# Kernel tuning notes

Hardware: AMD Instinct MI355X
Metric: run time of the kernel (lower is better)

## Reference

```python
import jax, jax.numpy as jnp
import numpy as np

N_NODES = 20000
N_EDGES = 320000
N_GRAPHS = 64
SEQ = 20
SCALAR = 16
EMB = 32
HID = 128
HEADS = 4
IN_DIM = SCALAR + 5 * EMB  # 176
NEG_SLOPE = 0.2


def masked_mean_embed(table, idx):
    # table: [V, EMB], idx: [N, L] with 0 = padding
    emb = table[idx]                                  # [N, L, EMB]
    mask = (idx != 0).astype(emb.dtype)[..., None]    # [N, L, 1]
    return (emb * mask).sum(axis=1) / (mask.sum(axis=1) + 1e-9)


def gat_conv(x, src, dst, W, att_src, att_dst, bias, heads, out_ch):
    # PyG GATConv (add_self_loops already applied to src/dst), concat heads.
    N = x.shape[0]
    xw = (x @ W).reshape(N, heads, out_ch)            # [N, H, C]
    a_src = (xw * att_src).sum(-1)                    # [N, H]
    a_dst = (xw * att_dst).sum(-1)                    # [N, H]
    e = jax.nn.leaky_relu(a_src[src] + a_dst[dst], NEG_SLOPE)  # [E, H]
    e_max = jax.ops.segment_max(e, dst, num_segments=N)
    e_max = jnp.where(jnp.isfinite(e_max), e_max, 0.0)
    ex = jnp.exp(e - e_max[dst])                      # [E, H]
    denom = jax.ops.segment_sum(ex, dst, num_segments=N)
    alpha = ex / (denom[dst] + 1e-16)                 # [E, H]
    msg = xw[src] * alpha[:, :, None]                 # [E, H, C]
    out = jax.ops.segment_sum(msg, dst, num_segments=N)
    return out.reshape(N, heads * out_ch) + bias


def setup_inputs() -> dict:
    key = jax.random.key(0)
    ks = jax.random.split(key, 24)
    s = 0.05
    inp = {
        "x_scalar": jax.random.normal(ks[0], (N_NODES, SCALAR), jnp.float32),
        "x_opcode": jax.random.randint(ks[1], (N_NODES, SEQ), 0, 256),
        "x_source": jax.random.randint(ks[2], (N_NODES, SEQ), 0, 512),
        "x_sink": jax.random.randint(ks[3], (N_NODES, SEQ), 0, 512),
        "x_string_manip": jax.random.randint(ks[4], (N_NODES, SEQ), 0, 128),
        "x_payload": jax.random.randint(ks[5], (N_NODES, SEQ), 0, 1024),
        "edge_index": jax.random.randint(ks[6], (2, N_EDGES), 0, N_NODES),
        "batch": jnp.sort(jax.random.randint(ks[7], (N_NODES,), 0, N_GRAPHS)),
        # embedding tables (row 0 = padding; masked out anyway)
        "emb_opcode": jax.random.normal(ks[8], (256, EMB)) * s,
        "emb_source": jax.random.normal(ks[9], (512, EMB)) * s,
        "emb_sink": jax.random.normal(ks[10], (512, EMB)) * s,
        "emb_string": jax.random.normal(ks[11], (128, EMB)) * s,
        "emb_payload": jax.random.normal(ks[12], (1024, EMB)) * s,
        "ln_gamma": jnp.ones((IN_DIM,), jnp.float32),
        "ln_beta": jnp.zeros((IN_DIM,), jnp.float32),
        "W1": jax.random.normal(ks[13], (IN_DIM, HEADS * HID)) * s,
        "att_src1": jax.random.normal(ks[14], (HEADS, HID)) * s,
        "att_dst1": jax.random.normal(ks[15], (HEADS, HID)) * s,
        "b1": jnp.zeros((HEADS * HID,), jnp.float32),
        "W2": jax.random.normal(ks[16], (HEADS * HID, HID)) * s,
        "att_src2": jax.random.normal(ks[17], (1, HID)) * s,
        "att_dst2": jax.random.normal(ks[18], (1, HID)) * s,
        "b2": jnp.zeros((HID,), jnp.float32),
        "cls_w1": jax.random.normal(ks[19], (HID, HID // 2)) * s,
        "cls_b1": jnp.zeros((HID // 2,), jnp.float32),
        "cls_w2": jax.random.normal(ks[20], (HID // 2, 2)) * s,
        "cls_b2": jnp.zeros((2,), jnp.float32),
    }
    return inp


def reference(x_scalar, x_opcode, x_source, x_sink, x_string_manip, x_payload,
              edge_index, batch,
              emb_opcode, emb_source, emb_sink, emb_string, emb_payload,
              ln_gamma, ln_beta,
              W1, att_src1, att_dst1, b1,
              W2, att_src2, att_dst2, b2,
              cls_w1, cls_b1, cls_w2, cls_b2):
    feats = jnp.concatenate([
        x_scalar,
        masked_mean_embed(emb_opcode, x_opcode),
        masked_mean_embed(emb_source, x_source),
        masked_mean_embed(emb_sink, x_sink),
        masked_mean_embed(emb_string, x_string_manip),
        masked_mean_embed(emb_payload, x_payload),
    ], axis=1)  # [N, 176]
    mu = feats.mean(-1, keepdims=True)
    var = ((feats - mu) ** 2).mean(-1, keepdims=True)
    h = (feats - mu) / jnp.sqrt(var + 1e-5) * ln_gamma + ln_beta

    # add self loops (PyG GATConv default)
    loops = jnp.arange(N_NODES, dtype=edge_index.dtype)
    src = jnp.concatenate([edge_index[0], loops])
    dst = jnp.concatenate([edge_index[1], loops])

    x = jax.nn.elu(gat_conv(h, src, dst, W1, att_src1, att_dst1, b1, HEADS, HID))
    x = jax.nn.elu(gat_conv(x, src, dst, W2, att_src2, att_dst2, b2, 1, HID))

    pooled = jax.ops.segment_max(x, batch, num_segments=N_GRAPHS)  # [G, HID]
    hcls = jax.nn.relu(pooled @ cls_w1 + cls_b1)
    return hcls @ cls_w2 + cls_b2  # [G, 2]
```

## Files before the change

### kernel.cpp

```cpp
#include <hip/hip_runtime.h>
#include <hip/hip_bf16.h>
#include <math.h>

#define N_NODES 20000
#define N_EDGES 320000
#define N_GRAPHS 64
#define SEQ 20
#define SCALAR 16
#define EMB 32
#define HID 128
#define IN_DIM 176
#define TOT_EDGES (N_EDGES + N_NODES)
#define CHUNK_SMALL 10000
#define POOL_SLICES 32

typedef _Float16 half8v __attribute__((ext_vector_type(8)));
typedef float f32x4 __attribute__((ext_vector_type(4)));
#define LO_SCALE 2048.0f
#define LO_INV (1.0f / 2048.0f)

#define PB2_ELEMS (16 * 8 * 64 * 8)
#define PB1_ELEMS (4 * 6 * 8 * 64 * 8)

__device__ inline float readlane_f(float v, int l) {
  return __uint_as_float(__builtin_amdgcn_readlane(__float_as_uint(v), l));
}
__device__ inline int readlane_i(int v, int l) {
  return __builtin_amdgcn_readlane(v, l);
}
__device__ inline float leaky(float e) { return e >= 0.f ? e : 0.2f * e; }
__device__ inline float elu(float v) { return v > 0.f ? v : expf(v) - 1.f; }

__global__ __launch_bounds__(256) void wasd_kernel(
    const float* __restrict__ W1, const float* __restrict__ att_s,
    const float* __restrict__ att_d, float* __restrict__ was4,
    float* __restrict__ wad4) {
  int lane = threadIdx.x & 63;
  int k = blockIdx.x * 4 + (threadIdx.x >> 6);
  if (k >= IN_DIM) return;
  const float* wrow = W1 + (size_t)k * 512;
  float s[4], d[4];
#pragma unroll
  for (int hh = 0; hh < 4; ++hh) {
    float w0 = wrow[hh * 128 + lane], w1 = wrow[hh * 128 + 64 + lane];
    float a0 = att_s[hh * 128 + lane], a1 = att_s[hh * 128 + 64 + lane];
    float c0 = att_d[hh * 128 + lane], c1 = att_d[hh * 128 + 64 + lane];
    s[hh] = w0 * a0 + w1 * a1;
    d[hh] = w0 * c0 + w1 * c1;
  }
  for (int off = 1; off < 64; off <<= 1) {
#pragma unroll
    for (int hh = 0; hh < 4; ++hh) {
      s[hh] += __shfl_xor(s[hh], off);
      d[hh] += __shfl_xor(d[hh], off);
    }
  }
  if (lane == 0) {
    *(float4*)&was4[k * 4] = make_float4(s[0], s[1], s[2], s[3]);
    *(float4*)&wad4[k * 4] = make_float4(d[0], d[1], d[2], d[3]);
  }
}

__global__ __launch_bounds__(256) void feats_ln_kernel(
    const float* __restrict__ xs,
    const int* __restrict__ i0, const int* __restrict__ i1,
    const int* __restrict__ i2, const int* __restrict__ i3,
    const int* __restrict__ i4,
    const float* __restrict__ t0, const float* __restrict__ t1,
    const float* __restrict__ t2, const float* __restrict__ t3,
    const float* __restrict__ t4,
    const float* __restrict__ gamma, const float* __restrict__ beta,
    const float* __restrict__ was4, const float* __restrict__ wad4,
    float* __restrict__ hout, float* __restrict__ a_s,
    float* __restrict__ a_d) {
  int lane = threadIdx.x & 63;
  int w = threadIdx.x >> 6;
  int n = blockIdx.x * 4 + w;
  if (n >= N_NODES) return;
  __shared__ int sidx[4][100];
  {
    int j = lane;
    int tab = j / 20, l = j - tab * 20;
    const int* ip = tab == 0 ? i0 : tab == 1 ? i1 : tab == 2 ? i2 : i3;
    sidx[w][j] = ip[n * SEQ + l];
    if (lane < 36) {
      int j2 = 64 + lane;
      int tab2 = j2 / 20, l2 = j2 - tab2 * 20;
      const int* ip2 = tab2 == 3 ? i3 : i4;
      sidx[w][j2] = ip2[n * SEQ + l2];
    }
  }
  bool l48 = lane < 48;
  float f0, f1, f2 = 0.f;
  if (lane < SCALAR) {
    f0 = xs[n * SCALAR + lane];
  } else {
    int tt = lane - SCALAR, tab = tt >> 5, d = tt & 31;
    const float* tp = tab == 0 ? t0 : t1;
    float sum = 0.f, cnt = 0.f;
#pragma unroll
    for (int l = 0; l < SEQ; ++l) {
      int id = sidx[w][tab * 20 + l];
      if (id != 0) { sum += tp[id * EMB + d]; cnt += 1.f; }
    }
    f0 = sum / (cnt + 1e-9f);
  }
  {
    int tt = 48 + lane, tab = tt >> 5, d = tt & 31;
    const float* tp = tab == 1 ? t1 : tab == 2 ? t2 : t3;
    float sum = 0.f, cnt = 0.f;
#pragma unroll
    for (int l = 0; l < SEQ; ++l) {
      int id = sidx[w][tab * 20 + l];
      if (id != 0) { sum += tp[id * EMB + d]; cnt += 1.f; }
    }
    f1 = sum / (cnt + 1e-9f);
  }
  if (l48) {
    int tt = 112 + lane, tab = tt >> 5, d = tt & 31;
    const float* tp = tab == 3 ? t3 : t4;
    float sum = 0.f, cnt = 0.f;
#pragma unroll
    for (int l = 0; l < SEQ; ++l) {
      int id = sidx[w][tab * 20 + l];
      if (id != 0) { sum += tp[id * EMB + d]; cnt += 1.f; }
    }
    f2 = sum / (cnt + 1e-9f);
  }
  float s = f0 + f1 + f2;
  for (int off = 1; off < 64; off <<= 1) s += __shfl_xor(s, off);
  float mu = s / (float)IN_DIM;
  float v = (f0 - mu) * (f0 - mu) + (f1 - mu) * (f1 - mu) +
            (l48 ? (f2 - mu) * (f2 - mu) : 0.f);
  for (int off = 1; off < 64; off <<= 1) v += __shfl_xor(v, off);
  float rstd = 1.0f / sqrtf(v / (float)IN_DIM + 1e-5f);
  float hv0 = (f0 - mu) * rstd * gamma[lane] + beta[lane];
  float hv1 = (f1 - mu) * rstd * gamma[64 + lane] + beta[64 + lane];
  float hv2 = l48 ? (f2 - mu) * rstd * gamma[128 + lane] + beta[128 + lane] : 0.f;
  float* hr = hout + (size_t)n * IN_DIM;
  hr[lane] = hv0;
  hr[64 + lane] = hv1;
  if (l48) hr[128 + lane] = hv2;

  const float4* wsv = (const float4*)was4;
  const float4* wdv = (const float4*)wad4;
  float4 wsa = wsv[lane], wsb = wsv[64 + lane];
  float4 wsc = l48 ? wsv[128 + lane] : make_float4(0.f, 0.f, 0.f, 0.f);
  float4 wda = wdv[lane], wdb = wdv[64 + lane];
  float4 wdc = l48 ? wdv[128 + lane] : make_float4(0.f, 0.f, 0.f, 0.f);
  float ps0 = hv0 * wsa.x + hv1 * wsb.x + hv2 * wsc.x;
  float ps1 = hv0 * wsa.y + hv1 * wsb.y + hv2 * wsc.y;
  float ps2 = hv0 * wsa.z + hv1 * wsb.z + hv2 * wsc.z;
  float ps3 = hv0 * wsa.w + hv1 * wsb.w + hv2 * wsc.w;
  float pd0 = hv0 * wda.x + hv1 * wdb.x + hv2 * wdc.x;
  float pd1 = hv0 * wda.y + hv1 * wdb.y + hv2 * wdc.y;
  float pd2 = hv0 * wda.z + hv1 * wdb.z + hv2 * wdc.z;
  float pd3 = hv0 * wda.w + hv1 * wdb.w + hv2 * wdc.w;
  for (int off = 1; off < 64; off <<= 1) {
    ps0 += __shfl_xor(ps0, off); ps1 += __shfl_xor(ps1, off);
    ps2 += __shfl_xor(ps2, off); ps3 += __shfl_xor(ps3, off);
    pd0 += __shfl_xor(pd0, off); pd1 += __shfl_xor(pd1, off);
    pd2 += __shfl_xor(pd2, off); pd3 += __shfl_xor(pd3, off);
  }
  if (lane == 0) {
    *(float4*)&a_s[n * 4] = make_float4(ps0, ps1, ps2, ps3);
    *(float4*)&a_d[n * 4] = make_float4(pd0, pd1, pd2, pd3);
  }
}

__global__ void count_kernel(const int* __restrict__ edge_index,
                             int* __restrict__ cnt, int E, int N) {
  int i = blockIdx.x * blockDim.x + threadIdx.x;
  if (i < E) {
    atomicAdd(&cnt[edge_index[E + i]], 1);
  } else if (i < E + N) {
    atomicAdd(&cnt[i - E], 1);
  }
}

__global__ __launch_bounds__(256) void prefix_kernel(const int* __restrict__ cnt,
                                                     int* __restrict__ indptr,
                                                     int n, int total) {
  __shared__ int ssum[256];
  int t = threadIdx.x;
  int per = (n + 255) / 256;
  int beg = t * per, end = min(beg + per, n);
  int s = 0;
  for (int i = beg; i < end; ++i) s += cnt[i];
  ssum[t] = s;
  __syncthreads();
  if (t == 0) {
    int run = 0;
    for (int i = 0; i < 256; ++i) { int v = ssum[i]; ssum[i] = run; run += v; }
  }
  __syncthreads();
  int run = ssum[t];
  for (int i = beg; i < end; ++i) { indptr[i] = run; run += cnt[i]; }
  if (t == 0) indptr[n] = total;
}

__global__ void scatter_kernel(const int* __restrict__ edge_index,
                               const int* __restrict__ indptr,
                               int* __restrict__ cursor,
                               int* __restrict__ srcs, int E, int N) {
  int i = blockIdx.x * blockDim.x + threadIdx.x;
  int s, d;
  if (i < E) { s = edge_index[i]; d = edge_index[E + i]; }
  else if (i < E + N) { s = i - E; d = s; }
  else return;
  int pos = indptr[d] + atomicAdd(&cursor[d], 1);
  srcs[pos] = s;
}

__global__ __launch_bounds__(256) void agg1h_kernel(
    const float* __restrict__ h, const float* __restrict__ a_src,
    const float* __restrict__ a_dst, const int* __restrict__ indptr,
    const int* __restrict__ srcs, float* __restrict__ aggh,
    int n0, int nM) {
  int lane = threadIdx.x & 63;
  int ln = blockIdx.x * 4 + (threadIdx.x >> 6);
  if (ln >= nM) return;
  int n = n0 + ln;
  int beg = indptr[n], end = indptr[n + 1];
  int deg = end - beg;
  float4 ad = *(const float4*)&a_dst[n * 4];
  bool l48 = lane < 48;
  float acc[4][3] = {};

  auto body = [&](int s, float al0, float al1, float al2, float al3) {
    const float* r = h + (size_t)s * IN_DIM;
    float v0 = r[lane];
    float v1 = r[64 + lane];
    float v2 = l48 ? r[128 + lane] : 0.f;
    acc[0][0] += al0 * v0; acc[0][1] += al0 * v1; acc[0][2] += al0 * v2;
    acc[1][0] += al1 * v0; acc[1][1] += al1 * v1; acc[1][2] += al1 * v2;
    acc[2][0] += al2 * v0; acc[2][1] += al2 * v1; acc[2][2] += al2 * v2;
    acc[3][0] += al3 * v0; acc[3][1] += al3 * v1; acc[3][2] += al3 * v2;
  };

  if (deg <= 64) {
    int j = beg + lane;
    int s = 0;
    float e0 = -INFINITY, e1 = -INFINITY, e2 = -INFINITY, e3 = -INFINITY;
    if (j < end) {
      s = srcs[j];
      float4 as = *(const float4*)&a_src[s * 4];
      e0 = leaky(as.x + ad.x); e1 = leaky(as.y + ad.y);
      e2 = leaky(as.z + ad.z); e3 = leaky(as.w + ad.w);
    }
    float m0 = e0, m1 = e1, m2 = e2, m3 = e3;
    for (int off = 1; off < 64; off <<= 1) {
      m0 = fmaxf(m0, __shfl_xor(m0, off)); m1 = fmaxf(m1, __shfl_xor(m1, off));
      m2 = fmaxf(m2, __shfl_xor(m2, off)); m3 = fmaxf(m3, __shfl_xor(m3, off));
    }
    float x0 = (j < end) ? expf(e0 - m0) : 0.f;
    float x1 = (j < end) ? expf(e1 - m1) : 0.f;
    float x2 = (j < end) ? expf(e2 - m2) : 0.f;
    float x3 = (j < end) ? expf(e3 - m3) : 0.f;
    float d0 = x0, d1 = x1, d2 = x2, d3 = x3;
    for (int off = 1; off < 64; off <<= 1) {
      d0 += __shfl_xor(d0, off); d1 += __shfl_xor(d1, off);
      d2 += __shfl_xor(d2, off); d3 += __shfl_xor(d3, off);
    }
    float al0 = x0 / (d0 + 1e-16f), al1 = x1 / (d1 + 1e-16f);
    float al2 = x2 / (d2 + 1e-16f), al3 = x3 / (d3 + 1e-16f);
    int jj = 0;
    for (; jj + 2 <= deg; jj += 2) {
      int sa = readlane_i(s, jj), sb = readlane_i(s, jj + 1);
      float a0 = readlane_f(al0, jj), a1 = readlane_f(al1, jj);
      float a2 = readlane_f(al2, jj), a3 = readlane_f(al3, jj);
      float b0 = readlane_f(al0, jj + 1), b1 = readlane_f(al1, jj + 1);
      float b2 = readlane_f(al2, jj + 1), b3 = readlane_f(al3, jj + 1);
      body(sa, a0, a1, a2, a3);
      body(sb, b0, b1, b2, b3);
    }
    if (jj < deg) {
      int sa = readlane_i(s, jj);
      body(sa, readlane_f(al0, jj), readlane_f(al1, jj),
           readlane_f(al2, jj), readlane_f(al3, jj));
    }
  } else {
    float m0 = -INFINITY, m1 = -INFINITY, m2 = -INFINITY, m3 = -INFINITY;
    for (int j0 = beg; j0 < end; j0 += 64) {
      int j = j0 + lane;
      if (j < end) {
        int s = srcs[j];
        float4 as = *(const float4*)&a_src[s * 4];
        m0 = fmaxf(m0, leaky(as.x + ad.x)); m1 = fmaxf(m1, leaky(as.y + ad.y));
        m2 = fmaxf(m2, leaky(as.z + ad.z)); m3 = fmaxf(m3, leaky(as.w + ad.w));
      }
    }
    for (int off = 1; off < 64; off <<= 1) {
      m0 = fmaxf(m0, __shfl_xor(m0, off)); m1 = fmaxf(m1, __shfl_xor(m1, off));
      m2 = fmaxf(m2, __shfl_xor(m2, off)); m3 = fmaxf(m3, __shfl_xor(m3, off));
    }
    float d0 = 0.f, d1 = 0.f, d2 = 0.f, d3 = 0.f;
    for (int j0 = beg; j0 < end; j0 += 64) {
      int j = j0 + lane;
      if (j < end) {
        int s = srcs[j];
        float4 as = *(const float4*)&a_src[s * 4];
        d0 += expf(leaky(as.x + ad.x) - m0); d1 += expf(leaky(as.y + ad.y) - m1);
        d2 += expf(leaky(as.z + ad.z) - m2); d3 += expf(leaky(as.w + ad.w) - m3);
      }
    }
    for (int off = 1; off < 64; off <<= 1) {
      d0 += __shfl_xor(d0, off); d1 += __shfl_xor(d1, off);
      d2 += __shfl_xor(d2, off); d3 += __shfl_xor(d3, off);
    }
    float r0 = 1.f / (d0 + 1e-16f), r1 = 1.f / (d1 + 1e-16f);
    float r2 = 1.f / (d2 + 1e-16f), r3 = 1.f / (d3 + 1e-16f);
    for (int j0 = beg; j0 < end; j0 += 64) {
      int jn = min(64, end - j0);
      int j = j0 + lane;
      int s = 0;
      float al0 = 0.f, al1 = 0.f, al2 = 0.f, al3 = 0.f;
      if (j < end) {
        s = srcs[j];
        float4 as = *(const float4*)&a_src[s * 4];
        al0 = expf(leaky(as.x + ad.x) - m0) * r0;
        al1 = expf(leaky(as.y + ad.y) - m1) * r1;
        al2 = expf(leaky(as.z + ad.z) - m2) * r2;
        al3 = expf(leaky(as.w + ad.w) - m3) * r3;
      }
      for (int jj = 0; jj < jn; ++jj) {
        body(readlane_i(s, jj), readlane_f(al0, jj), readlane_f(al1, jj),
             readlane_f(al2, jj), readlane_f(al3, jj));
      }
    }
  }

  size_t base = (size_t)ln * (4 * IN_DIM);
#pragma unroll
  for (int hh = 0; hh < 4; ++hh) {
    aggh[base + hh * IN_DIM + lane] = acc[hh][0];
    aggh[base + hh * IN_DIM + 64 + lane] = acc[hh][1];
    if (l48) aggh[base + hh * IN_DIM + 128 + lane] = acc[hh][2];
  }
}

__global__ __launch_bounds__(256) void pack_w2_kernel(
    const float* __restrict__ W2, _Float16* __restrict__ PBh,
    _Float16* __restrict__ PBl) {
  int t = blockIdx.x * 256 + threadIdx.x;
  int lane = t & 63, wi = t >> 6;
  int r = lane & 15, g = lane >> 4;
  int ks = wi >> 3, ntile = wi & 7;
  int col = ntile * 16 + r;
  size_t o = ((size_t)wi * 64 + lane) * 8;
#pragma unroll
  for (int j = 0; j < 8; ++j) {
    int k = ks * 32 + g * 8 + j;
    float v = W2[(size_t)k * 128 + col];
    _Float16 h = (_Float16)v;
    PBh[o + j] = h;
    PBl[o + j] = (_Float16)((v - (float)h) * LO_SCALE);
  }
}

__global__ __launch_bounds__(256) void pack_w1_kernel(
    const float* __restrict__ W1, _Float16* __restrict__ PBh,
    _Float16* __restrict__ PBl) {
  int t = blockIdx.x * 256 + threadIdx.x;
  int lane = t & 63, wi = t >> 6;
  int r = lane & 15, g = lane >> 4;
  int ntile = wi & 7, rem = wi >> 3;
  int ks = rem % 6, hh = rem / 6;
  int col = hh * 128 + ntile * 16 + r;
  size_t o = ((size_t)wi * 64 + lane) * 8;
#pragma unroll
  for (int j = 0; j < 8; ++j) {
    int k = ks * 32 + g * 8 + j;
    float v = (k < IN_DIM) ? W1[(size_t)k * 512 + col] : 0.f;
    _Float16 h = (_Float16)v;
    PBh[o + j] = h;
    PBl[o + j] = (_Float16)((v - (float)h) * LO_SCALE);
  }
}

__global__ __launch_bounds__(256) void gemm_head_mfma_kernel(
    const float* __restrict__ aggh, const half8v* __restrict__ PBh,
    const half8v* __restrict__ PBl, const float* __restrict__ b1,
    float* __restrict__ out1, int M, int n0) {
  int lane = threadIdx.x & 63;
  int wid = (blockIdx.x * 256 + threadIdx.x) >> 6;
  int colhalf = wid & 1;
  int hh = (wid >> 1) & 3;
  int rg = wid >> 3;
  int rows0 = rg * 32;
  if (rows0 >= M) return;
  int r = lane & 15, g = lane >> 4;
  f32x4 acc[2][4] = {};
  f32x4 accm[2][4] = {};
  const float* a0 = aggh + ((size_t)(rows0 + r) * 4 + hh) * IN_DIM;
  const float* a1 = aggh + ((size_t)(rows0 + 16 + r) * 4 + hh) * IN_DIM;
#pragma unroll 2
  for (int ks = 0; ks < 6; ++ks) {
    int kg = ks * 32 + g * 8;
    int koff = (kg + 8 <= IN_DIM) ? kg : 0;
    half8v ah[2], al[2];
#pragma unroll
    for (int mt = 0; mt < 2; ++mt) {
      const float* ap = (mt ? a1 : a0) + koff;
      float av[8];
      *(float4*)&av[0] = *(const float4*)(ap);
      *(float4*)&av[4] = *(const float4*)(ap + 4);
#pragma unroll
      for (int j = 0; j < 8; ++j) {
        _Float16 hv = (_Float16)av[j];
        ah[mt][j] = hv;
        al[mt][j] = (_Float16)((av[j] - (float)hv) * LO_SCALE);
      }
    }
    const half8v* bh = PBh + (size_t)(((hh * 6 + ks) * 8 + colhalf * 4) * 64) + lane;
    const half8v* bl = PBl + (size_t)(((hh * 6 + ks) * 8 + colhalf * 4) * 64) + lane;
#pragma unroll
    for (int nt = 0; nt < 4; ++nt) {
      half8v bhv = bh[nt * 64], blv = bl[nt * 64];
#pragma unroll
      for (int mt = 0; mt < 2; ++mt) {
        accm[mt][nt] = __builtin_amdgcn_mfma_f32_16x16x32_f16(al[mt], bhv, accm[mt][nt], 0, 0, 0);
        accm[mt][nt] = __builtin_amdgcn_mfma_f32_16x16x32_f16(ah[mt], blv, accm[mt][nt], 0, 0, 0);
        acc[mt][nt]  = __builtin_amdgcn_mfma_f32_16x16x32_f16(ah[mt], bhv, acc[mt][nt], 0, 0, 0);
      }
    }
  }
#pragma unroll
  for (int nt = 0; nt < 4; ++nt) {
    int col = hh * 128 + colhalf * 64 + nt * 16 + r;
    float bb = b1[col];
#pragma unroll
    for (int mt = 0; mt < 2; ++mt) {
#pragma unroll
      for (int i = 0; i < 4; ++i) {
        int row = rows0 + mt * 16 + g * 4 + i;
        if (row < M)
          out1[(size_t)(n0 + row) * 512 + col] =
              elu(acc[mt][nt][i] + accm[mt][nt][i] * LO_INV + bb);
      }
    }
  }
}

__global__ __launch_bounds__(256) void gemm2att_mfma_kernel(
    const float* __restrict__ A, const half8v* __restrict__ PBh,
    const half8v* __restrict__ PBl, const float* __restrict__ att_s,
    const float* __restrict__ att_d, float* __restrict__ C,
    float* __restrict__ a_s, float* __restrict__ a_d, int M) {
  int lane = threadIdx.x & 63;
  int wid = (blockIdx.x * 256 + threadIdx.x) >> 6;
  int colhalf = wid & 1;
  int rg = wid >> 1;
  int row0 = rg * 16;
  if (row0 >= M) return;
  int r = lane & 15, g = lane >> 4;
  const float* arow = A + (size_t)(row0 + r) * 512 + g * 8;
  f32x4 acc[4] = {};
  f32x4 accm[4] = {};
#pragma unroll 2
  for (int ks = 0; ks < 16; ++ks) {
    float av[8];
    *(float4*)&av[0] = *(const float4*)(arow + ks * 32);
    *(float4*)&av[4] = *(const float4*)(arow + ks * 32 + 4);
    half8v ah, al;
#pragma unroll
    for (int j = 0; j < 8; ++j) {
      _Float16 hv = (_Float16)av[j];
      ah[j] = hv;
      al[j] = (_Float16)((av[j] - (float)hv) * LO_SCALE);
    }
    const half8v* bh = PBh + (size_t)((ks * 8 + colhalf * 4) * 64) + lane;
    const half8v* bl = PBl + (size_t)((ks * 8 + colhalf * 4) * 64) + lane;
#pragma unroll
    for (int nt = 0; nt < 4; ++nt) {
      half8v bhv = bh[nt * 64], blv = bl[nt * 64];
      accm[nt] = __builtin_amdgcn_mfma_f32_16x16x32_f16(al, bhv, accm[nt], 0, 0, 0);
      accm[nt] = __builtin_amdgcn_mfma_f32_16x16x32_f16(ah, blv, accm[nt], 0, 0, 0);
      acc[nt]  = __builtin_amdgcn_mfma_f32_16x16x32_f16(ah, bhv, acc[nt], 0, 0, 0);
    }
  }
  float ps[4] = {0.f, 0.f, 0.f, 0.f}, pd[4] = {0.f, 0.f, 0.f, 0.f};
#pragma unroll
  for (int nt = 0; nt < 4; ++nt) {
    int col = colhalf * 64 + nt * 16 + r;
    float as_ = att_s[col], ad_ = att_d[col];
#pragma unroll
    for (int i = 0; i < 4; ++i) {
      float v = acc[nt][i] + accm[nt][i] * LO_INV;
      int row = row0 + g * 4 + i;
      C[(size_t)row * 128 + col] = v;
      ps[i] += v * as_;
      pd[i] += v * ad_;
    }
  }
#pragma unroll
  for (int i = 0; i < 4; ++i) {
    for (int off = 1; off < 16; off <<= 1) {
      ps[i] += __shfl_xor(ps[i], off);
      pd[i] += __shfl_xor(pd[i], off);
    }
  }
  if (r == 0) {
#pragma unroll
    for (int i = 0; i < 4; ++i) {
      atomicAdd(&a_s[row0 + g * 4 + i], ps[i]);
      atomicAdd(&a_d[row0 + g * 4 + i], pd[i]);
    }
  }
}

__global__ __launch_bounds__(256) void agg2_kernel(
    const float* __restrict__ xw, const float* __restrict__ a_src,
    const float* __restrict__ a_dst, const int* __restrict__ indptr,
    const int* __restrict__ srcs, const float* __restrict__ bias,
    float* __restrict__ out) {
  int lane = threadIdx.x & 63;
  int n = blockIdx.x * 4 + (threadIdx.x >> 6);
  if (n >= N_NODES) return;
  int beg = indptr[n], end = indptr[n + 1];
  int deg = end - beg;
  float adn = a_dst[n];
  int half = lane >> 5, l32 = lane & 31;
  float4 acc = make_float4(0.f, 0.f, 0.f, 0.f);

  auto pairs = [&](int s, float al, int jn) {
    int jj = 0;
    for (; jj + 2 <= jn; jj += 2) {
      int sa = readlane_i(s, jj), sb = readlane_i(s, jj + 1);
      float aa = readlane_f(al, jj), ab = readlane_f(al, jj + 1);
      int sh = half ? sb : sa;
      float ahx = half ? ab : aa;
      float4 v = *(const float4*)&xw[(size_t)sh * HID + l32 * 4];
      acc.x += ahx * v.x; acc.y += ahx * v.y; acc.z += ahx * v.z; acc.w += ahx * v.w;
    }
    if (jj < jn) {
      int sa = readlane_i(s, jj);
      float ahx = half ? 0.f : readlane_f(al, jj);
      float4 v = *(const float4*)&xw[(size_t)sa * HID + l32 * 4];
      acc.x += ahx * v.x; acc.y += ahx * v.y; acc.z += ahx * v.z; acc.w += ahx * v.w;
    }
  };

  if (deg <= 64) {
    int j = beg + lane;
    int s = 0;
    float e = -INFINITY;
    if (j < end) { s = srcs[j]; e = leaky(a_src[s] + adn); }
    float m = e;
    for (int off = 1; off < 64; off <<= 1) m = fmaxf(m, __shfl_xor(m, off));
    float x = (j < end) ? expf(e - m) : 0.f;
    float d = x;
    for (int off = 1; off < 64; off <<= 1) d += __shfl_xor(d, off);
    float al = x / (d + 1e-16f);
    pairs(s, al, deg);
  } else {
    float m = -INFINITY;
    for (int j0 = beg; j0 < end; j0 += 64) {
      int j = j0 + lane;
      if (j < end) m = fmaxf(m, leaky(a_src[srcs[j]] + adn));
    }
    for (int off = 1; off < 64; off <<= 1) m = fmaxf(m, __shfl_xor(m, off));
    float d = 0.f;
    for (int j0 = beg; j0 < end; j0 += 64) {
      int j = j0 + lane;
      if (j < end) d += expf(leaky(a_src[srcs[j]] + adn) - m);
    }
    for (int off = 1; off < 64; off <<= 1) d += __shfl_xor(d, off);
    float rd = 1.f / (d + 1e-16f);
    for (int j0 = beg; j0 < end; j0 += 64) {
      int jn = min(64, end - j0);
      int j = j0 + lane;
      int s = 0;
      float al = 0.f;
      if (j < end) {
        s = srcs[j];
        al = expf(leaky(a_src[s] + adn) - m) * rd;
      }
      pairs(s, al, jn);
    }
  }

  acc.x += __shfl_xor(acc.x, 32); acc.y += __shfl_xor(acc.y, 32);
  acc.z += __shfl_xor(acc.z, 32); acc.w += __shfl_xor(acc.w, 32);
  if (half == 0) {
    float4 b = *(const float4*)&bias[l32 * 4];
    float4 o;
    o.x = elu(acc.x + b.x); o.y = elu(acc.y + b.y);
    o.z = elu(acc.z + b.z); o.w = elu(acc.w + b.w);
    *(float4*)&out[(size_t)n * HID + l32 * 4] = o;
  }
}

__global__ void gstart_kernel(const int* __restrict__ batch,
                              int* __restrict__ gstarts, int N, int G) {
  int t = threadIdx.x;
  if (t > G) return;
  int lo = 0, hi = N;
  while (lo < hi) {
    int mid = (lo + hi) >> 1;
    if (batch[mid] < t) lo = mid + 1; else hi = mid;
  }
  gstarts[t] = lo;
}

__global__ __launch_bounds__(HID) void pool_part_kernel(
    const float* __restrict__ out2, const int* __restrict__ gstarts,
    float* __restrict__ part) {
  int g = blockIdx.x, s = blockIdx.y, t = threadIdx.x;
  int beg = gstarts[g], end = gstarts[g + 1];
  int len = end - beg;
  int b0 = beg + (int)(((long long)len * s) / POOL_SLICES);
  int b1 = beg + (int)(((long long)len * (s + 1)) / POOL_SLICES);
  float m = -INFINITY;
  for (int n = b0; n < b1; ++n) m = fmaxf(m, out2[(size_t)n * HID + t]);
  part[((size_t)g * POOL_SLICES + s) * HID + t] = m;
}

__global__ __launch_bounds__(HID) void pool_reduce_kernel(
    const float* __restrict__ part, float* __restrict__ pooled) {
  int g = blockIdx.x, t = threadIdx.x;
  float m = -INFINITY;
#pragma unroll
  for (int s = 0; s < POOL_SLICES; ++s)
    m = fmaxf(m, part[((size_t)g * POOL_SLICES + s) * HID + t]);
  pooled[g * HID + t] = m;
}

__global__ __launch_bounds__(HID) void cls_kernel(const float* __restrict__ pooled,
                                                  const float* __restrict__ w1,
                                                  const float* __restrict__ b1,
                                                  const float* __restrict__ w2,
                                                  const float* __restrict__ b2,
                                                  float* __restrict__ out) {
  int g = blockIdx.x, t = threadIdx.x;
  __shared__ float sp[HID], sh1[HID / 2];
  sp[t] = pooled[g * HID + t];
  __syncthreads();
  if (t < HID / 2) {
    float s = b1[t];
    for (int k = 0; k < HID; ++k) s += sp[k] * w1[k * (HID / 2) + t];
    sh1[t] = fmaxf(s, 0.f);
  }
  __syncthreads();
  if (t < 2) {
    float o = b2[t];
    for (int k = 0; k < HID / 2; ++k) o += sh1[k] * w2[k * 2 + t];
    out[g * 2 + t] = o;
  }
}

extern "C" void kernel_launch(void* const* d_in, const int* in_sizes, int n_in,
                              void* d_out, int out_size, void* d_ws, size_t ws_size,
                              hipStream_t stream) {
  const float* x_scalar = (const float*)d_in[0];
  const int* x_opcode   = (const int*)d_in[1];
  const int* x_source   = (const int*)d_in[2];
  const int* x_sink     = (const int*)d_in[3];
  const int* x_string   = (const int*)d_in[4];
  const int* x_payload  = (const int*)d_in[5];
  const int* edge_index = (const int*)d_in[6];
  const int* batch      = (const int*)d_in[7];
  const float* emb_opcode = (const float*)d_in[8];
  const float* emb_source = (const float*)d_in[9];
  const float* emb_sink   = (const float*)d_in[10];
  const float* emb_string = (const float*)d_in[11];
  const float* emb_payload= (const float*)d_in[12];
  const float* ln_gamma = (const float*)d_in[13];
  const float* ln_beta  = (const float*)d_in[14];
  const float* W1       = (const float*)d_in[15];
  const float* att_src1 = (const float*)d_in[16];
  const float* att_dst1 = (const float*)d_in[17];
  const float* b1       = (const float*)d_in[18];
  const float* W2       = (const float*)d_in[19];
  const float* att_src2 = (const float*)d_in[20];
  const float* att_dst2 = (const float*)d_in[21];
  const float* b2       = (const float*)d_in[22];
  const float* cls_w1   = (const float*)d_in[23];
  const float* cls_b1   = (const float*)d_in[24];
  const float* cls_w2   = (const float*)d_in[25];
  const float* cls_b2   = (const float*)d_in[26];

  auto total_bytes = [&](int chunk) -> size_t {
    size_t f = (size_t)N_NODES * IN_DIM + (size_t)chunk * 4 * IN_DIM +
               (size_t)N_NODES * 512 + (size_t)N_NODES * HID +
               N_NODES * 4 * 2 + N_NODES * 2 + IN_DIM * 4 * 2 + N_GRAPHS * HID;
    size_t ii = (N_NODES + 1) + N_NODES * 2 + TOT_EDGES + (N_GRAPHS + 1);
    size_t f16b = (size_t)2 * (PB2_ELEMS + PB1_ELEMS) * sizeof(_Float16) + 32;
    size_t poolb = (size_t)N_GRAPHS * POOL_SLICES * HID * 4 + 32;
    return f * 4 + ii * 4 + f16b + poolb + 256;
  };
  int chunk = (ws_size >= total_bytes(N_NODES)) ? N_NODES : CHUNK_SMALL;

  float* h      = (float*)d_ws;
  float* aggh   = h + (size_t)N_NODES * IN_DIM;
  float* out1   = aggh + (size_t)chunk * 4 * IN_DIM;
  float* out2   = out1 + (size_t)N_NODES * 512;
  float* a1s    = out2 + (size_t)N_NODES * HID;
  float* a1d    = a1s + N_NODES * 4;
  float* was4   = a1d + N_NODES * 4;
  float* wad4   = was4 + IN_DIM * 4;
  float* pooled = wad4 + IN_DIM * 4;
  int* indptr = (int*)(pooled + N_GRAPHS * HID);
  int* cnt    = indptr + (N_NODES + 1);
  int* cursor = cnt + N_NODES;
  float* a2s  = (float*)(cursor + N_NODES);
  float* a2d  = a2s + N_NODES;
  int* srcs   = (int*)(a2d + N_NODES);
  int* gstarts= srcs + TOT_EDGES;
  uintptr_t pal = ((uintptr_t)(gstarts + N_GRAPHS + 1) + 15) & ~(uintptr_t)15;
  _Float16* PB2h = (_Float16*)pal;
  _Float16* PB2l = PB2h + PB2_ELEMS;
  _Float16* PB1h = PB2l + PB2_ELEMS;
  _Float16* PB1l = PB1h + PB1_ELEMS;
  uintptr_t ppal = ((uintptr_t)(PB1l + PB1_ELEMS) + 15) & ~(uintptr_t)15;
  float* pool_part = (float*)ppal;
  float* xw2  = h;

  hipMemsetAsync(cnt, 0, 4 * N_NODES * sizeof(int), stream);

  const int NB4 = (N_NODES + 3) / 4;

  wasd_kernel<<<(IN_DIM + 3) / 4, 256, 0, stream>>>(W1, att_src1, att_dst1, was4, wad4);

  feats_ln_kernel<<<NB4, 256, 0, stream>>>(
      x_scalar, x_opcode, x_source, x_sink, x_string, x_payload,
      emb_opcode, emb_source, emb_sink, emb_string, emb_payload,
      ln_gamma, ln_beta, was4, wad4, h, a1s, a1d);

  int nthreads = TOT_EDGES;
  count_kernel<<<(nthreads + 255) / 256, 256, 0, stream>>>(edge_index, cnt, N_EDGES, N_NODES);
  prefix_kernel<<<1, 256, 0, stream>>>(cnt, indptr, N_NODES, TOT_EDGES);
  scatter_kernel<<<(nthreads + 255) / 256, 256, 0, stream>>>(edge_index, indptr, cursor, srcs, N_EDGES, N_NODES);

  pack_w1_kernel<<<48, 256, 0, stream>>>(W1, PB1h, PB1l);
  pack_w2_kernel<<<32, 256, 0, stream>>>(W2, PB2h, PB2l);

  for (int n0 = 0; n0 < N_NODES; n0 += chunk) {
    int nM = min(chunk, N_NODES - n0);
    agg1h_kernel<<<(nM + 3) / 4, 256, 0, stream>>>(h, a1s, a1d, indptr, srcs, aggh, n0, nM);
    int rgs = (nM + 31) / 32;
    gemm_head_mfma_kernel<<<rgs * 2, 256, 0, stream>>>(
        aggh, (const half8v*)PB1h, (const half8v*)PB1l, b1, out1, nM, n0);
  }

  gemm2att_mfma_kernel<<<((N_NODES + 15) / 16 * 2 + 3) / 4, 256, 0, stream>>>(
      out1, (const half8v*)PB2h, (const half8v*)PB2l, att_src2, att_dst2,
      xw2, a2s, a2d, N_NODES);

  agg2_kernel<<<NB4, 256, 0, stream>>>(xw2, a2s, a2d, indptr, srcs, b2, out2);

  gstart_kernel<<<1, 128, 0, stream>>>(batch, gstarts, N_NODES, N_GRAPHS);
  pool_part_kernel<<<dim3(N_GRAPHS, POOL_SLICES), HID, 0, stream>>>(out2, gstarts, pool_part);
  pool_reduce_kernel<<<N_GRAPHS, HID, 0, stream>>>(pool_part, pooled);
  cls_kernel<<<N_GRAPHS, HID, 0, stream>>>(pooled, cls_w1, cls_b1, cls_w2, cls_b2, (float*)d_out);
}
```

Baseline: 390.8 us.

## Merge setup kernels, parallelize prefix scan, and shrink GEMM wave tiles

```diff
diff --git a/kernel.cpp b/kernel.cpp
--- a/kernel.cpp
+++ b/kernel.cpp
@@ -31,33 +31,69 @@
 __device__ inline float leaky(float e) { return e >= 0.f ? e : 0.2f * e; }
 __device__ inline float elu(float v) { return v > 0.f ? v : expf(v) - 1.f; }
 
-__global__ __launch_bounds__(256) void wasd_kernel(
-    const float* __restrict__ W1, const float* __restrict__ att_s,
-    const float* __restrict__ att_d, float* __restrict__ was4,
-    float* __restrict__ wad4) {
-  int lane = threadIdx.x & 63;
-  int k = blockIdx.x * 4 + (threadIdx.x >> 6);
-  if (k >= IN_DIM) return;
-  const float* wrow = W1 + (size_t)k * 512;
-  float s[4], d[4];
-#pragma unroll
-  for (int hh = 0; hh < 4; ++hh) {
-    float w0 = wrow[hh * 128 + lane], w1 = wrow[hh * 128 + 64 + lane];
-    float a0 = att_s[hh * 128 + lane], a1 = att_s[hh * 128 + 64 + lane];
-    float c0 = att_d[hh * 128 + lane], c1 = att_d[hh * 128 + 64 + lane];
-    s[hh] = w0 * a0 + w1 * a1;
-    d[hh] = w0 * c0 + w1 * c1;
-  }
-  for (int off = 1; off < 64; off <<= 1) {
+__global__ __launch_bounds__(256) void setup_kernel(
+    const float* __restrict__ W1, const float* __restrict__ att_s1,
+    const float* __restrict__ att_d1, const float* __restrict__ W2,
+    float* __restrict__ was4, float* __restrict__ wad4,
+    _Float16* __restrict__ PB1h, _Float16* __restrict__ PB1l,
+    _Float16* __restrict__ PB2h, _Float16* __restrict__ PB2l) {
+  int b = blockIdx.x;
+  if (b < 44) {
+    int lane = threadIdx.x & 63;
+    int k = b * 4 + (threadIdx.x >> 6);
+    if (k >= IN_DIM) return;
+    const float* wrow = W1 + (size_t)k * 512;
+    float s[4], d[4];
 #pragma unroll
     for (int hh = 0; hh < 4; ++hh) {
-      s[hh] += __shfl_xor(s[hh], off);
-      d[hh] += __shfl_xor(d[hh], off);
-    }
-  }
-  if (lane == 0) {
-    *(float4*)&was4[k * 4] = make_float4(s[0], s[1], s[2], s[3]);
-    *(float4*)&wad4[k * 4] = make_float4(d[0], d[1], d[2], d[3]);
+      float w0 = wrow[hh * 128 + lane], w1 = wrow[hh * 128 + 64 + lane];
+      float a0 = att_s1[hh * 128 + lane], a1 = att_s1[hh * 128 + 64 + lane];
+      float c0 = att_d1[hh * 128 + lane], c1 = att_d1[hh * 128 + 64 + lane];
+      s[hh] = w0 * a0 + w1 * a1;
+      d[hh] = w0 * c0 + w1 * c1;
+    }
+    for (int off = 1; off < 64; off <<= 1) {
+#pragma unroll
+      for (int hh = 0; hh < 4; ++hh) {
+        s[hh] += __shfl_xor(s[hh], off);
+        d[hh] += __shfl_xor(d[hh], off);
+      }
+    }
+    if (lane == 0) {
+      *(float4*)&was4[k * 4] = make_float4(s[0], s[1], s[2], s[3]);
+      *(float4*)&wad4[k * 4] = make_float4(d[0], d[1], d[2], d[3]);
+    }
+  } else if (b < 92) {
+    int t = (b - 44) * 256 + threadIdx.x;
+    int lane = t & 63, wi = t >> 6;
+    int r = lane & 15, g = lane >> 4;
+    int ntile = wi & 7, rem = wi >> 3;
+    int ks = rem % 6, hh = rem / 6;
+    int col = hh * 128 + ntile * 16 + r;
+    size_t o = ((size_t)wi * 64 + lane) * 8;
+#pragma unroll
+    for (int j = 0; j < 8; ++j) {
+      int k = ks * 32 + g * 8 + j;
+      float v = (k < IN_DIM) ? W1[(size_t)k * 512 + col] : 0.f;
+      _Float16 h = (_Float16)v;
+      PB1h[o + j] = h;
+      PB1l[o + j] = (_Float16)((v - (float)h) * LO_SCALE);
+    }
+  } else {
+    int t = (b - 92) * 256 + threadIdx.x;
+    int lane = t & 63, wi = t >> 6;
+    int r = lane & 15, g = lane >> 4;
+    int ks = wi >> 3, ntile = wi & 7;
+    int col = ntile * 16 + r;
+    size_t o = ((size_t)wi * 64 + lane) * 8;
+#pragma unroll
+    for (int j = 0; j < 8; ++j) {
+      int k = ks * 32 + g * 8 + j;
+      float v = W2[(size_t)k * 128 + col];
+      _Float16 h = (_Float16)v;
+      PB2h[o + j] = h;
+      PB2l[o + j] = (_Float16)((v - (float)h) * LO_SCALE);
+    }
   }
 }
 
@@ -178,23 +214,24 @@
   }
 }
 
-__global__ __launch_bounds__(256) void prefix_kernel(const int* __restrict__ cnt,
-                                                     int* __restrict__ indptr,
-                                                     int n, int total) {
-  __shared__ int ssum[256];
+__global__ __launch_bounds__(1024) void prefix_kernel(const int* __restrict__ cnt,
+                                                      int* __restrict__ indptr,
+                                                      int n, int total) {
+  __shared__ int ss[1024];
   int t = threadIdx.x;
-  int per = (n + 255) / 256;
+  int per = (n + 1023) / 1024;
   int beg = t * per, end = min(beg + per, n);
   int s = 0;
   for (int i = beg; i < end; ++i) s += cnt[i];
-  ssum[t] = s;
+  ss[t] = s;
   __syncthreads();
-  if (t == 0) {
-    int run = 0;
-    for (int i = 0; i < 256; ++i) { int v = ssum[i]; ssum[i] = run; run += v; }
-  }
-  __syncthreads();
-  int run = ssum[t];
+  for (int off = 1; off < 1024; off <<= 1) {
+    int v = (t >= off) ? ss[t - off] : 0;
+    __syncthreads();
+    ss[t] += v;
+    __syncthreads();
+  }
+  int run = ss[t] - s;
   for (int i = beg; i < end; ++i) { indptr[i] = run; run += cnt[i]; }
   if (t == 0) indptr[n] = total;
 }
@@ -339,45 +376,6 @@
   }
 }
 
-__global__ __launch_bounds__(256) void pack_w2_kernel(
-    const float* __restrict__ W2, _Float16* __restrict__ PBh,
-    _Float16* __restrict__ PBl) {
-  int t = blockIdx.x * 256 + threadIdx.x;
-  int lane = t & 63, wi = t >> 6;
-  int r = lane & 15, g = lane >> 4;
-  int ks = wi >> 3, ntile = wi & 7;
-  int col = ntile * 16 + r;
-  size_t o = ((size_t)wi * 64 + lane) * 8;
-#pragma unroll
-  for (int j = 0; j < 8; ++j) {
-    int k = ks * 32 + g * 8 + j;
-    float v = W2[(size_t)k * 128 + col];
-    _Float16 h = (_Float16)v;
-    PBh[o + j] = h;
-    PBl[o + j] = (_Float16)((v - (float)h) * LO_SCALE);
-  }
-}
-
-__global__ __launch_bounds__(256) void pack_w1_kernel(
-    const float* __restrict__ W1, _Float16* __restrict__ PBh,
-    _Float16* __restrict__ PBl) {
-  int t = blockIdx.x * 256 + threadIdx.x;
-  int lane = t & 63, wi = t >> 6;
-  int r = lane & 15, g = lane >> 4;
-  int ntile = wi & 7, rem = wi >> 3;
-  int ks = rem % 6, hh = rem / 6;
-  int col = hh * 128 + ntile * 16 + r;
-  size_t o = ((size_t)wi * 64 + lane) * 8;
-#pragma unroll
-  for (int j = 0; j < 8; ++j) {
-    int k = ks * 32 + g * 8 + j;
-    float v = (k < IN_DIM) ? W1[(size_t)k * 512 + col] : 0.f;
-    _Float16 h = (_Float16)v;
-    PBh[o + j] = h;
-    PBl[o + j] = (_Float16)((v - (float)h) * LO_SCALE);
-  }
-}
-
 __global__ __launch_bounds__(256) void gemm_head_mfma_kernel(
     const float* __restrict__ aggh, const half8v* __restrict__ PBh,
     const half8v* __restrict__ PBl, const float* __restrict__ b1,
@@ -387,42 +385,35 @@
   int colhalf = wid & 1;
   int hh = (wid >> 1) & 3;
   int rg = wid >> 3;
-  int rows0 = rg * 32;
+  int rows0 = rg * 16;
   if (rows0 >= M) return;
   int r = lane & 15, g = lane >> 4;
-  f32x4 acc[2][4] = {};
-  f32x4 accm[2][4] = {};
+  f32x4 acc[4] = {};
+  f32x4 accm[4] = {};
   const float* a0 = aggh + ((size_t)(rows0 + r) * 4 + hh) * IN_DIM;
-  const float* a1 = aggh + ((size_t)(rows0 + 16 + r) * 4 + hh) * IN_DIM;
 #pragma unroll 2
   for (int ks = 0; ks < 6; ++ks) {
     int kg = ks * 32 + g * 8;
     int koff = (kg + 8 <= IN_DIM) ? kg : 0;
-    half8v ah[2], al[2];
-#pragma unroll
-    for (int mt = 0; mt < 2; ++mt) {
-      const float* ap = (mt ? a1 : a0) + koff;
-      float av[8];
-      *(float4*)&av[0] = *(const float4*)(ap);
-      *(float4*)&av[4] = *(const float4*)(ap + 4);
-#pragma unroll
-      for (int j = 0; j < 8; ++j) {
-        _Float16 hv = (_Float16)av[j];
-        ah[mt][j] = hv;
-        al[mt][j] = (_Float16)((av[j] - (float)hv) * LO_SCALE);
-      }
+    const float* ap = a0 + koff;
+    float av[8];
+    *(float4*)&av[0] = *(const float4*)(ap);
+    *(float4*)&av[4] = *(const float4*)(ap + 4);
+    half8v ah, al;
+#pragma unroll
+    for (int j = 0; j < 8; ++j) {
+      _Float16 hv = (_Float16)av[j];
+      ah[j] = hv;
+      al[j] = (_Float16)((av[j] - (float)hv) * LO_SCALE);
     }
     const half8v* bh = PBh + (size_t)(((hh * 6 + ks) * 8 + colhalf * 4) * 64) + lane;
     const half8v* bl = PBl + (size_t)(((hh * 6 + ks) * 8 + colhalf * 4) * 64) + lane;
 #pragma unroll
     for (int nt = 0; nt < 4; ++nt) {
       half8v bhv = bh[nt * 64], blv = bl[nt * 64];
-#pragma unroll
-      for (int mt = 0; mt < 2; ++mt) {
-        accm[mt][nt] = __builtin_amdgcn_mfma_f32_16x16x32_f16(al[mt], bhv, accm[mt][nt], 0, 0, 0);
-        accm[mt][nt] = __builtin_amdgcn_mfma_f32_16x16x32_f16(ah[mt], blv, accm[mt][nt], 0, 0, 0);
-        acc[mt][nt]  = __builtin_amdgcn_mfma_f32_16x16x32_f16(ah[mt], bhv, acc[mt][nt], 0, 0, 0);
-      }
+      accm[nt] = __builtin_amdgcn_mfma_f32_16x16x32_f16(al, bhv, accm[nt], 0, 0, 0);
+      accm[nt] = __builtin_amdgcn_mfma_f32_16x16x32_f16(ah, blv, accm[nt], 0, 0, 0);
+      acc[nt]  = __builtin_amdgcn_mfma_f32_16x16x32_f16(ah, bhv, acc[nt], 0, 0, 0);
     }
   }
 #pragma unroll
@@ -430,14 +421,11 @@
     int col = hh * 128 + colhalf * 64 + nt * 16 + r;
     float bb = b1[col];
 #pragma unroll
-    for (int mt = 0; mt < 2; ++mt) {
-#pragma unroll
-      for (int i = 0; i < 4; ++i) {
-        int row = rows0 + mt * 16 + g * 4 + i;
-        if (row < M)
-          out1[(size_t)(n0 + row) * 512 + col] =
-              elu(acc[mt][nt][i] + accm[mt][nt][i] * LO_INV + bb);
-      }
+    for (int i = 0; i < 4; ++i) {
+      int row = rows0 + g * 4 + i;
+      if (row < M)
+        out1[(size_t)(n0 + row) * 512 + col] =
+            elu(acc[nt][i] + accm[nt][i] * LO_INV + bb);
     }
   }
 }
@@ -449,14 +437,14 @@
     float* __restrict__ a_s, float* __restrict__ a_d, int M) {
   int lane = threadIdx.x & 63;
   int wid = (blockIdx.x * 256 + threadIdx.x) >> 6;
-  int colhalf = wid & 1;
-  int rg = wid >> 1;
+  int colq = wid & 3;
+  int rg = wid >> 2;
   int row0 = rg * 16;
   if (row0 >= M) return;
   int r = lane & 15, g = lane >> 4;
   const float* arow = A + (size_t)(row0 + r) * 512 + g * 8;
-  f32x4 acc[4] = {};
-  f32x4 accm[4] = {};
+  f32x4 acc[2] = {};
+  f32x4 accm[2] = {};
 #pragma unroll 2
   for (int ks = 0; ks < 16; ++ks) {
     float av[8];
@@ -469,10 +457,10 @@
       ah[j] = hv;
       al[j] = (_Float16)((av[j] - (float)hv) * LO_SCALE);
     }
-    const half8v* bh = PBh + (size_t)((ks * 8 + colhalf * 4) * 64) + lane;
-    const half8v* bl = PBl + (size_t)((ks * 8 + colhalf * 4) * 64) + lane;
-#pragma unroll
-    for (int nt = 0; nt < 4; ++nt) {
+    const half8v* bh = PBh + (size_t)((ks * 8 + colq * 2) * 64) + lane;
+    const half8v* bl = PBl + (size_t)((ks * 8 + colq * 2) * 64) + lane;
+#pragma unroll
+    for (int nt = 0; nt < 2; ++nt) {
       half8v bhv = bh[nt * 64], blv = bl[nt * 64];
       accm[nt] = __builtin_amdgcn_mfma_f32_16x16x32_f16(al, bhv, accm[nt], 0, 0, 0);
       accm[nt] = __builtin_amdgcn_mfma_f32_16x16x32_f16(ah, blv, accm[nt], 0, 0, 0);
@@ -481,8 +469,8 @@
   }
   float ps[4] = {0.f, 0.f, 0.f, 0.f}, pd[4] = {0.f, 0.f, 0.f, 0.f};
 #pragma unroll
-  for (int nt = 0; nt < 4; ++nt) {
-    int col = colhalf * 64 + nt * 16 + r;
+  for (int nt = 0; nt < 2; ++nt) {
+    int col = colq * 32 + nt * 16 + r;
     float as_ = att_s[col], ad_ = att_d[col];
 #pragma unroll
     for (int i = 0; i < 4; ++i) {
@@ -720,7 +708,8 @@
 
   const int NB4 = (N_NODES + 3) / 4;
 
-  wasd_kernel<<<(IN_DIM + 3) / 4, 256, 0, stream>>>(W1, att_src1, att_dst1, was4, wad4);
+  setup_kernel<<<124, 256, 0, stream>>>(W1, att_src1, att_dst1, W2,
+                                        was4, wad4, PB1h, PB1l, PB2h, PB2l);
 
   feats_ln_kernel<<<NB4, 256, 0, stream>>>(
       x_scalar, x_opcode, x_source, x_sink, x_string, x_payload,
@@ -729,21 +718,18 @@
 
   int nthreads = TOT_EDGES;
   count_kernel<<<(nthreads + 255) / 256, 256, 0, stream>>>(edge_index, cnt, N_EDGES, N_NODES);
-  prefix_kernel<<<1, 256, 0, stream>>>(cnt, indptr, N_NODES, TOT_EDGES);
+  prefix_kernel<<<1, 1024, 0, stream>>>(cnt, indptr, N_NODES, TOT_EDGES);
   scatter_kernel<<<(nthreads + 255) / 256, 256, 0, stream>>>(edge_index, indptr, cursor, srcs, N_EDGES, N_NODES);
-
-  pack_w1_kernel<<<48, 256, 0, stream>>>(W1, PB1h, PB1l);
-  pack_w2_kernel<<<32, 256, 0, stream>>>(W2, PB2h, PB2l);
 
   for (int n0 = 0; n0 < N_NODES; n0 += chunk) {
     int nM = min(chunk, N_NODES - n0);
     agg1h_kernel<<<(nM + 3) / 4, 256, 0, stream>>>(h, a1s, a1d, indptr, srcs, aggh, n0, nM);
-    int rgs = (nM + 31) / 32;
+    int rgs = (nM + 15) / 16;
     gemm_head_mfma_kernel<<<rgs * 2, 256, 0, stream>>>(
         aggh, (const half8v*)PB1h, (const half8v*)PB1l, b1, out1, nM, n0);
   }
 
-  gemm2att_mfma_kernel<<<((N_NODES + 15) / 16 * 2 + 3) / 4, 256, 0, stream>>>(
+  gemm2att_mfma_kernel<<<(N_NODES + 15) / 16, 256, 0, stream>>>(
       out1, (const half8v*)PB2h, (const half8v*)PB2l, att_src2, att_dst2,
       xw2, a2s, a2d, N_NODES);
 
```

Measured after the change: 382.0 us. 1.02x faster.
